# Optimization experiments

Measured on AMD Instinct MI355X. Metric: run time of the kernel, lower is better.

The kernel has to match this reference:

```python
import jax, jax.numpy as jnp
import numpy as np

EMB_DIM = 2048
N_Q_HEADS = 32
N_KV_HEADS = 8
HEAD_DIM = EMB_DIM // N_Q_HEADS  # 64
N_REP = N_Q_HEADS // N_KV_HEADS  # 4
ROPE_BASE = 10000.0


def setup_inputs() -> dict:
    key = jax.random.key(0)
    ks = jax.random.split(key, 9)
    B, T = 2, 2048
    kv_dim = HEAD_DIM * N_KV_HEADS
    s = 0.02
    return {
        "x":  jax.random.normal(ks[0], (B, T, EMB_DIM), jnp.float32),
        "Wq": jax.random.normal(ks[1], (EMB_DIM, EMB_DIM), jnp.float32) * s,
        "bq": jax.random.normal(ks[2], (EMB_DIM,), jnp.float32) * s,
        "Wk": jax.random.normal(ks[3], (kv_dim, EMB_DIM), jnp.float32) * s,
        "bk": jax.random.normal(ks[4], (kv_dim,), jnp.float32) * s,
        "Wv": jax.random.normal(ks[5], (kv_dim, EMB_DIM), jnp.float32) * s,
        "bv": jax.random.normal(ks[6], (kv_dim,), jnp.float32) * s,
        "Wo": jax.random.normal(ks[7], (EMB_DIM, EMB_DIM), jnp.float32) * s,
        "bo": jax.random.normal(ks[8], (EMB_DIM,), jnp.float32) * s,
    }


def _rope_tables(T, D, dtype):
    inv_freq = 1.0 / (ROPE_BASE ** (jnp.arange(0, D, 2, dtype=jnp.float32) / D))
    t = jnp.arange(T, dtype=jnp.float32)
    freqs = jnp.einsum("i,j->ij", t, inv_freq)          # [T, D/2]
    emb = jnp.concatenate([freqs, freqs], axis=-1)       # [T, D]
    # broadcast over batch and heads: [1, T, 1, D]
    return jnp.cos(emb)[None, :, None, :].astype(dtype), jnp.sin(emb)[None, :, None, :].astype(dtype)


def _rotate_half(x):
    x1, x2 = jnp.split(x, 2, axis=-1)
    return jnp.concatenate([-x2, x1], axis=-1)


def reference(x, Wq, bq, Wk, bk, Wv, bv, Wo, bo):
    B, T, C = x.shape
    q = (x @ Wq.T + bq).reshape(B, T, N_Q_HEADS, HEAD_DIM)
    k = (x @ Wk.T + bk).reshape(B, T, N_KV_HEADS, HEAD_DIM)
    v = (x @ Wv.T + bv).reshape(B, T, N_KV_HEADS, HEAD_DIM)

    cos, sin = _rope_tables(T, HEAD_DIM, x.dtype)
    q = q * cos + _rotate_half(q) * sin
    k = k * cos + _rotate_half(k) * sin

    q = q.transpose(0, 2, 1, 3)                          # [B, Hq, T, D]
    k = k.transpose(0, 2, 1, 3)                          # [B, Hkv, T, D]
    v = v.transpose(0, 2, 1, 3)
    # GQA: repeat_interleave kv heads to match query heads
    k = jnp.repeat(k, N_REP, axis=1)                     # [B, Hq, T, D]
    v = jnp.repeat(v, N_REP, axis=1)

    scale = 1.0 / jnp.sqrt(jnp.asarray(HEAD_DIM, x.dtype))
    att = jnp.einsum("bhqd,bhkd->bhqk", q, k) * scale    # [B, Hq, T, T]
    causal = jnp.tril(jnp.ones((T, T), dtype=bool))
    att = jnp.where(causal[None, None], att, -jnp.inf)
    att = jax.nn.softmax(att, axis=-1)

    y = jnp.einsum("bhqk,bhkd->bhqd", att, v)            # [B, Hq, T, D]
    y = y.transpose(0, 2, 1, 3).reshape(B, T, C)
    return y @ Wo.T + bo
```

## Files before the change

### kernel.cpp

```cpp
#include <hip/hip_runtime.h>
#include <hip/hip_bf16.h>
#include <math.h>


typedef __attribute__((ext_vector_type(8))) short short8;
typedef __attribute__((ext_vector_type(4))) float f32x4;

#define MFMA16(a,b,c) __builtin_amdgcn_mfma_f32_16x16x32_bf16((a),(b),(c),0,0,0)
#define QSCALE 0.18033688011112043f
#define NFREQ  (-13.28771237954945f / 32.0f)

__device__ __forceinline__ ushort f2bf(float f) {
  union { float f; unsigned u; } x; x.f = f;
  unsigned r = x.u + 0x7fffu + ((x.u >> 16) & 1u);
  return (ushort)(r >> 16);
}
__device__ __forceinline__ uint pkbf(float a, float b) {
  union { float f; unsigned u; } x, y; x.f = a; y.f = b;
  return ((x.u + 0x8000u) >> 16) | ((y.u + 0x8000u) & 0xffff0000u);
}

__device__ __forceinline__ void g2l16(const void* g, void* l) {
  __builtin_amdgcn_global_load_lds(
      (__attribute__((address_space(1))) void*)g,
      (__attribute__((address_space(3))) void*)l, 16, 0, 0);
}

__global__ void cvt_all(const float* __restrict__ x,  const float* __restrict__ wq,
                        const float* __restrict__ wk, const float* __restrict__ wv,
                        const float* __restrict__ wo,
                        ushort* __restrict__ x_bf, ushort* __restrict__ wqkv,
                        ushort* __restrict__ wo_bf) {
  int i = blockIdx.x * 256 + threadIdx.x;
  const float4* src; ushort* dst; int off;
  if (i < 2097152)      { src = (const float4*)x;  dst = x_bf;             off = i; }
  else if (i < 3145728) { src = (const float4*)wq; dst = wqkv;             off = i - 2097152; }
  else if (i < 3407872) { src = (const float4*)wk; dst = wqkv + 4194304;   off = i - 3145728; }
  else if (i < 3670016) { src = (const float4*)wv; dst = wqkv + 5242880;   off = i - 3407872; }
  else                  { src = (const float4*)wo; dst = wo_bf;            off = i - 3670016; }
  float4 v = src[off];
  ushort4 o;
  o.x = f2bf(v.x); o.y = f2bf(v.y); o.z = f2bf(v.z); o.w = f2bf(v.w);
  ((ushort4*)dst)[off] = o;
}

__global__ __launch_bounds__(256, 3)
void gemm_qkv(const ushort* __restrict__ A, const ushort* __restrict__ Bw,
              const float* __restrict__ bq, const float* __restrict__ bk,
              const float* __restrict__ bv,
              ushort* __restrict__ qr, ushort* __restrict__ kr,
              ushort* __restrict__ vt) {
  const int K = 2048;
  __shared__ ushort As[2][128*32];
  __shared__ ushort Bs[2][128*32];
  const int tid = threadIdx.x;
  const int wave = tid >> 6, lane = tid & 63;
  const int wm = wave >> 1, wn = wave & 1;
  const int quad = lane >> 4, l16 = lane & 15;
  const int swg = (l16 >> 1) & 3;
  int id = blockIdx.y * 24 + blockIdx.x;
  id = (id & 7) * 96 + (id >> 3);
  const int bx = id % 24, by = id / 24;
  const int m0 = by * 128, n0 = bx * 128;

  f32x4 acc[4][4] = {};

  auto stage = [&](int buf, int k0) {
#pragma unroll
    for (int i = 0; i < 2; ++i) {
      int cbase = (i*4 + wave) * 64;
      int p = cbase + lane;
      int row = p >> 2, pcb = p & 3;
      int cl = pcb ^ ((row >> 1) & 3);
      g2l16(A  + (size_t)(m0 + row) * K + k0 + cl * 8, As[buf] + (size_t)cbase * 8);
      g2l16(Bw + (size_t)(n0 + row) * K + k0 + cl * 8, Bs[buf] + (size_t)cbase * 8);
    }
  };

  stage(0, 0);
  for (int k0 = 0; k0 < K; k0 += 32) {
    __syncthreads();
    int cur = (k0 >> 5) & 1;
    if (k0 + 32 < K) stage(cur ^ 1, k0 + 32);

    short8 af[4], bfr[4];
#pragma unroll
    for (int mi = 0; mi < 4; ++mi)
      af[mi] = *(const short8*)(As[cur] + (wm*64 + mi*16 + l16)*32 + ((quad ^ swg) * 8));
#pragma unroll
    for (int ni = 0; ni < 4; ++ni)
      bfr[ni] = *(const short8*)(Bs[cur] + (wn*64 + ni*16 + l16)*32 + ((quad ^ swg) * 8));
#pragma unroll
    for (int mi = 0; mi < 4; ++mi)
#pragma unroll
      for (int ni = 0; ni < 4; ++ni)
        acc[mi][ni] = MFMA16(af[mi], bfr[ni], acc[mi][ni]);
  }

  const int bb = m0 >> 11;
  const int tb = (m0 & 2047) + wm*64;

  if (bx < 20) {
    const bool isq = bx < 16;
    const float scale = isq ? QSCALE : 1.0f;
#pragma unroll
    for (int ni = 0; ni < 2; ++ni) {
      int n = n0 + wn*64 + ni*16 + l16;
      int d = ni*16 + l16;
      float bias1, bias2;
      ushort* dst;
      if (isq) {
        bias1 = bq[n]; bias2 = bq[n + 32];
        dst = qr + ((size_t)(bb*32 + (n >> 6)) * 2048) * 64 + d;
      } else {
        bias1 = bk[n - 2048]; bias2 = bk[n - 2016];
        dst = kr + ((size_t)(bb*8 + ((n >> 6) - 32)) * 2048) * 64 + d;
      }
      float invf = exp2f((float)d * NFREQ);
#pragma unroll
      for (int mi = 0; mi < 4; ++mi) {
#pragma unroll
        for (int r = 0; r < 4; ++r) {
          int t = tb + mi*16 + quad*4 + r;
          float x1 = acc[mi][ni][r]   + bias1;
          float x2 = acc[mi][ni+2][r] + bias2;
          float f = (float)t * invf;
          float sn = __sinf(f), cs = __cosf(f);
          dst[(size_t)t*64]      = f2bf((x1*cs - x2*sn) * scale);
          dst[(size_t)t*64 + 32] = f2bf((x2*cs + x1*sn) * scale);
        }
      }
    }
  } else {
#pragma unroll
    for (int ni = 0; ni < 4; ++ni) {
      int n = n0 + wn*64 + ni*16 + l16;
      int d = ni*16 + l16;
      float bias = bv[n - 2560];
      ushort* dst = vt + ((size_t)(bb*8 + ((n - 2560) >> 6)) * 64 + d) * 2048;
#pragma unroll
      for (int mi = 0; mi < 4; ++mi) {
        int t = tb + mi*16 + quad*4;
        uint2 pk;
        pk.x = (uint)f2bf(acc[mi][ni][0]+bias) | ((uint)f2bf(acc[mi][ni][1]+bias) << 16);
        pk.y = (uint)f2bf(acc[mi][ni][2]+bias) | ((uint)f2bf(acc[mi][ni][3]+bias) << 16);
        *(uint2*)(dst + t) = pk;
      }
    }
  }
}

__global__ __launch_bounds__(256, 3)
void gemm128(const ushort* __restrict__ A, const ushort* __restrict__ Bw,
             const float* __restrict__ b0,
             float* __restrict__ Cout, int M, int N, int K) {
  __shared__ ushort As[2][128*32];
  __shared__ ushort Bs[2][128*32];
  const int tid = threadIdx.x;
  const int wave = tid >> 6, lane = tid & 63;
  const int wm = wave >> 1, wn = wave & 1;
  const int quad = lane >> 4, l16 = lane & 15;
  const int swg = (l16 >> 1) & 3;
  int id = blockIdx.y * 16 + blockIdx.x;
  id = (id & 7) * 64 + (id >> 3);
  const int m0 = (id / 16) * 128, n0 = (id % 16) * 128;

  f32x4 acc[4][4] = {};

  auto stage = [&](int buf, int k0) {
#pragma unroll
    for (int i = 0; i < 2; ++i) {
      int cbase = (i*4 + wave) * 64;
      int p = cbase + lane;
      int row = p >> 2, pcb = p & 3;
      int cl = pcb ^ ((row >> 1) & 3);
      g2l16(A  + (size_t)(m0 + row) * K + k0 + cl * 8, As[buf] + (size_t)cbase * 8);
      g2l16(Bw + (size_t)(n0 + row) * K + k0 + cl * 8, Bs[buf] + (size_t)cbase * 8);
    }
  };

  stage(0, 0);
  for (int k0 = 0; k0 < K; k0 += 32) {
    __syncthreads();
    int cur = (k0 >> 5) & 1;
    if (k0 + 32 < K) stage(cur ^ 1, k0 + 32);

    short8 af[4], bfr[4];
#pragma unroll
    for (int mi = 0; mi < 4; ++mi)
      af[mi] = *(const short8*)(As[cur] + (wm*64 + mi*16 + l16)*32 + ((quad ^ swg) * 8));
#pragma unroll
    for (int ni = 0; ni < 4; ++ni)
      bfr[ni] = *(const short8*)(Bs[cur] + (wn*64 + ni*16 + l16)*32 + ((quad ^ swg) * 8));
#pragma unroll
    for (int mi = 0; mi < 4; ++mi)
#pragma unroll
      for (int ni = 0; ni < 4; ++ni)
        acc[mi][ni] = MFMA16(af[mi], bfr[ni], acc[mi][ni]);
  }

#pragma unroll
  for (int ni = 0; ni < 4; ++ni) {
    int n = n0 + wn*64 + ni*16 + l16;
    float bias = b0[n];
#pragma unroll
    for (int mi = 0; mi < 4; ++mi) {
#pragma unroll
      for (int r = 0; r < 4; ++r) {
        int m = m0 + wm*64 + mi*16 + quad*4 + r;
        Cout[(size_t)m * N + n] = acc[mi][ni][r] + bias;
      }
    }
  }
}

__global__ __launch_bounds__(512, 4)
void attn(const ushort* __restrict__ Q, const ushort* __restrict__ Kb,
          const ushort* __restrict__ Vt, ushort* __restrict__ Y) {
  __shared__ ushort Ks[2][64*64];
  __shared__ ushort Vs[2][64*64];
  __shared__ ushort Ps[8*16*64];
  const int tid = threadIdx.x, wave = tid >> 6, lane = tid & 63;
  const int quad = lane >> 4, l16 = lane & 15;
  const int h = blockIdx.y, b = blockIdx.z;
  const int hk = h >> 2;
  const ushort* Qb = Q  + ((size_t)(b*32 + h)  * 2048) * 64;
  const ushort* Kg = Kb + ((size_t)(b*8 + hk) * 2048) * 64;
  const ushort* Vg = Vt + ((size_t)(b*8 + hk) * 64) * 2048;
  ushort* Pw = Ps + wave * 1024;
  const int sw = l16 & 7;

  auto stage = [&](int buf, int kt) {
    int p = tid;
    int row = p >> 3, pcb = p & 7;
    int cl = pcb ^ (row & 7);
    g2l16(Kg + (size_t)(kt*64 + row)*64 + cl*8, Ks[buf] + wave*512);
    g2l16(Vg + (size_t)row*2048 + kt*64 + cl*8, Vs[buf] + wave*512);
  };

  for (int pass = 0; pass < 2; ++pass) {
    const int qt = pass ? (15 - blockIdx.x) : blockIdx.x;
    const int q0 = qt * 128;
    const int qrow = q0 + wave*16 + l16;
    short8 qf0 = *(const short8*)(Qb + (size_t)qrow*64 + quad*8);
    short8 qf1 = *(const short8*)(Qb + (size_t)qrow*64 + 32 + quad*8);

    f32x4 o[4] = {};
    f32x4 l4 = {0.f, 0.f, 0.f, 0.f};

    __syncthreads();
    stage(0, 0);

    const int ktmax = qt*2 + 1;
    for (int kt = 0; kt <= ktmax; ++kt) {
      __syncthreads();
      int cur = kt & 1;
      if (kt < ktmax) stage(cur ^ 1, kt + 1);

      f32x4 s[4];
      __builtin_amdgcn_s_setprio(1);
#pragma unroll
      for (int kb = 0; kb < 4; ++kb) {
        const ushort* krow = Ks[cur] + (kb*16 + l16)*64;
        short8 kf0 = *(const short8*)(krow + ((quad       ^ sw) * 8));
        short8 kf1 = *(const short8*)(krow + (((4 + quad) ^ sw) * 8));
        f32x4 z = {0.f, 0.f, 0.f, 0.f};
        z = MFMA16(kf0, qf0, z);
        s[kb] = MFMA16(kf1, qf1, z);
      }
      __builtin_amdgcn_s_setprio(0);

      if (kt >= qt*2) {
        int ql = q0 + wave*16 + l16;
#pragma unroll
        for (int kb = 0; kb < 4; ++kb) {
          int key = kt*64 + kb*16 + quad*4;
#pragma unroll
          for (int r = 0; r < 4; ++r)
            if (key + r > ql) s[kb][r] = -INFINITY;
        }
      }

#pragma unroll
      for (int kb = 0; kb < 4; ++kb)
#pragma unroll
        for (int r = 0; r < 4; ++r)
          s[kb][r] = __builtin_amdgcn_exp2f(s[kb][r]);

      l4 += (s[0] + s[1]) + (s[2] + s[3]);

#pragma unroll
      for (int kb = 0; kb < 4; ++kb) {
        uint2 pk;
        pk.x = pkbf(s[kb][0], s[kb][1]);
        pk.y = pkbf(s[kb][2], s[kb][3]);
        int G = (kb*2 + (quad >> 1)) ^ sw;
        *(uint2*)((char*)Pw + l16*128 + G*16 + (quad & 1)*8) = pk;
      }

      __builtin_amdgcn_s_setprio(1);
#pragma unroll
      for (int kc = 0; kc < 2; ++kc) {
        short8 pf = *(const short8*)((char*)Pw + l16*128 + (((kc*4 + quad) ^ sw) * 16));
#pragma unroll
        for (int db = 0; db < 4; ++db) {
          const ushort* vrow = Vs[cur] + (db*16 + l16)*64;
          short8 vf = *(const short8*)(vrow + (((kc*4 + quad) ^ sw) * 8));
          o[db] = MFMA16(vf, pf, o[db]);
        }
      }
      __builtin_amdgcn_s_setprio(0);
    }

    float l = (l4[0] + l4[1]) + (l4[2] + l4[3]);
    l += __shfl_xor(l, 16);
    l += __shfl_xor(l, 32);
    float inv = 1.0f / l;

    int q = q0 + wave*16 + l16;
#pragma unroll
    for (int db = 0; db < 4; ++db) {
      size_t base = ((size_t)(b*2048 + q)) * 2048 + h*64 + db*16 + quad*4;
      ((uint*)Y)[base >> 1]       = pkbf(o[db][0]*inv, o[db][1]*inv);
      ((uint*)Y)[(base >> 1) + 1] = pkbf(o[db][2]*inv, o[db][3]*inv);
    }
  }
}

extern "C" void kernel_launch(void* const* d_in, const int* in_sizes, int n_in,
                              void* d_out, int out_size, void* d_ws, size_t ws_size,
                              hipStream_t stream) {
  (void)in_sizes; (void)n_in; (void)out_size; (void)ws_size;
  const float* x  = (const float*)d_in[0];
  const float* Wq = (const float*)d_in[1];
  const float* bq = (const float*)d_in[2];
  const float* Wk = (const float*)d_in[3];
  const float* bk = (const float*)d_in[4];
  const float* Wv = (const float*)d_in[5];
  const float* bv = (const float*)d_in[6];
  const float* Wo = (const float*)d_in[7];
  const float* bo = (const float*)d_in[8];
  float* out = (float*)d_out;

  ushort* ws    = (ushort*)d_ws;
  ushort* x_bf  = ws;
  ushort* wqkv  = x_bf + 8388608;
  ushort* wo_bf = wqkv + 6291456;
  ushort* qr    = wo_bf + 4194304;
  ushort* kr    = qr + 8388608;
  ushort* vt    = kr + 2097152;
  ushort* Y     = x_bf;

  cvt_all<<<18432, 256, 0, stream>>>(x, Wq, Wk, Wv, Wo, x_bf, wqkv, wo_bf);
  gemm_qkv<<<dim3(24, 32), 256, 0, stream>>>(x_bf, wqkv, bq, bk, bv, qr, kr, vt);
  attn<<<dim3(8, 32, 2), 512, 0, stream>>>(qr, kr, vt, Y);
  gemm128<<<dim3(16, 32), 256, 0, stream>>>(Y, wo_bf, bo, out, 4096, 2048, 2048);
}
```

Measured before the change: 286.3 us.

## Switch attention to 32x32 MFMA tiles with in-register P via permlane32 swap

Changes the attention kernel from 16x16x32 MFMA with 8 waves of 16 query rows each to 32x32x16 MFMA with 4 waves of 32 query rows each. The P matrix is no longer written to and read back from LDS. It is repacked in registers with permlane32_swap so it can feed the PV MFMA directly. Removing the LDS round trip for P and using larger MFMA tiles should cut LDS traffic and instruction count. The costs are fewer threads per block, more registers per thread (f32x16 accumulators), and lower occupancy.

```diff
diff --git a/kernel.cpp b/kernel.cpp
--- a/kernel.cpp
+++ b/kernel.cpp
@@ -5,8 +5,11 @@
 
 typedef __attribute__((ext_vector_type(8))) short short8;
 typedef __attribute__((ext_vector_type(4))) float f32x4;
+typedef __attribute__((ext_vector_type(16))) float f32x16;
+typedef __attribute__((ext_vector_type(2))) unsigned int uint2v;
 
 #define MFMA16(a,b,c) __builtin_amdgcn_mfma_f32_16x16x32_bf16((a),(b),(c),0,0,0)
+#define MFMA32(a,b,c) __builtin_amdgcn_mfma_f32_32x32x16_bf16((a),(b),(c),0,0,0)
 #define QSCALE 0.18033688011112043f
 #define NFREQ  (-13.28771237954945f / 32.0f)
 
@@ -214,39 +217,41 @@
   }
 }
 
-__global__ __launch_bounds__(512, 4)
+__global__ __launch_bounds__(256, 2)
 void attn(const ushort* __restrict__ Q, const ushort* __restrict__ Kb,
           const ushort* __restrict__ Vt, ushort* __restrict__ Y) {
   __shared__ ushort Ks[2][64*64];
   __shared__ ushort Vs[2][64*64];
-  __shared__ ushort Ps[8*16*64];
   const int tid = threadIdx.x, wave = tid >> 6, lane = tid & 63;
-  const int quad = lane >> 4, l16 = lane & 15;
+  const int l32 = lane & 31, hh = lane >> 5;
   const int h = blockIdx.y, b = blockIdx.z;
   const int hk = h >> 2;
   const ushort* Qb = Q  + ((size_t)(b*32 + h)  * 2048) * 64;
   const ushort* Kg = Kb + ((size_t)(b*8 + hk) * 2048) * 64;
   const ushort* Vg = Vt + ((size_t)(b*8 + hk) * 64) * 2048;
-  ushort* Pw = Ps + wave * 1024;
-  const int sw = l16 & 7;
 
   auto stage = [&](int buf, int kt) {
-    int p = tid;
-    int row = p >> 3, pcb = p & 7;
-    int cl = pcb ^ (row & 7);
-    g2l16(Kg + (size_t)(kt*64 + row)*64 + cl*8, Ks[buf] + wave*512);
-    g2l16(Vg + (size_t)row*2048 + kt*64 + cl*8, Vs[buf] + wave*512);
+#pragma unroll
+    for (int i = 0; i < 2; ++i) {
+      int p = i*256 + tid;
+      int row = p >> 3, pcb = p & 7;
+      int cl = pcb ^ (row & 7);
+      g2l16(Kg + (size_t)(kt*64 + row)*64 + cl*8, Ks[buf] + (size_t)p*8);
+      g2l16(Vg + (size_t)row*2048 + kt*64 + cl*8, Vs[buf] + (size_t)p*8);
+    }
   };
 
   for (int pass = 0; pass < 2; ++pass) {
     const int qt = pass ? (15 - blockIdx.x) : blockIdx.x;
     const int q0 = qt * 128;
-    const int qrow = q0 + wave*16 + l16;
-    short8 qf0 = *(const short8*)(Qb + (size_t)qrow*64 + quad*8);
-    short8 qf1 = *(const short8*)(Qb + (size_t)qrow*64 + 32 + quad*8);
-
-    f32x4 o[4] = {};
-    f32x4 l4 = {0.f, 0.f, 0.f, 0.f};
+    const int qrow = q0 + wave*32 + l32;
+    short8 qf[4];
+#pragma unroll
+    for (int ks = 0; ks < 4; ++ks)
+      qf[ks] = *(const short8*)(Qb + (size_t)qrow*64 + ks*16 + hh*8);
+
+    f32x16 o[2] = {};
+    float lsum = 0.f;
 
     __syncthreads();
     stage(0, 0);
@@ -257,72 +262,81 @@
       int cur = kt & 1;
       if (kt < ktmax) stage(cur ^ 1, kt + 1);
 
-      f32x4 s[4];
+      f32x16 s[2];
       __builtin_amdgcn_s_setprio(1);
 #pragma unroll
-      for (int kb = 0; kb < 4; ++kb) {
-        const ushort* krow = Ks[cur] + (kb*16 + l16)*64;
-        short8 kf0 = *(const short8*)(krow + ((quad       ^ sw) * 8));
-        short8 kf1 = *(const short8*)(krow + (((4 + quad) ^ sw) * 8));
-        f32x4 z = {0.f, 0.f, 0.f, 0.f};
-        z = MFMA16(kf0, qf0, z);
-        s[kb] = MFMA16(kf1, qf1, z);
+      for (int kb = 0; kb < 2; ++kb) {
+        f32x16 z = {};
+#pragma unroll
+        for (int ks = 0; ks < 4; ++ks) {
+          int row = kb*32 + l32;
+          short8 kf = *(const short8*)(Ks[cur] + row*64 + (((ks*2 + hh) ^ (row & 7)) * 8));
+          z = MFMA32(kf, qf[ks], z);
+        }
+        s[kb] = z;
       }
       __builtin_amdgcn_s_setprio(0);
 
-      if (kt >= qt*2) {
-        int ql = q0 + wave*16 + l16;
-#pragma unroll
-        for (int kb = 0; kb < 4; ++kb) {
-          int key = kt*64 + kb*16 + quad*4;
-#pragma unroll
-          for (int r = 0; r < 4; ++r)
-            if (key + r > ql) s[kb][r] = -INFINITY;
+      if (kt*64 + 63 > qrow - l32) {
+#pragma unroll
+        for (int kb = 0; kb < 2; ++kb)
+#pragma unroll
+          for (int r = 0; r < 16; ++r) {
+            int key = kt*64 + kb*32 + (r & 3) + 8*(r >> 2) + 4*hh;
+            if (key > qrow) s[kb][r] = -INFINITY;
+          }
+      }
+
+#pragma unroll
+      for (int kb = 0; kb < 2; ++kb)
+#pragma unroll
+        for (int r = 0; r < 16; ++r) {
+          s[kb][r] = __builtin_amdgcn_exp2f(s[kb][r]);
+          lsum += s[kb][r];
         }
-      }
-
-#pragma unroll
-      for (int kb = 0; kb < 4; ++kb)
-#pragma unroll
-        for (int r = 0; r < 4; ++r)
-          s[kb][r] = __builtin_amdgcn_exp2f(s[kb][r]);
-
-      l4 += (s[0] + s[1]) + (s[2] + s[3]);
-
-#pragma unroll
-      for (int kb = 0; kb < 4; ++kb) {
+
+      __builtin_amdgcn_s_setprio(1);
+#pragma unroll
+      for (int kb = 0; kb < 2; ++kb) {
+#pragma unroll
+        for (int c = 0; c < 2; ++c) {
+          int rb = c*8;
+          uint a0 = pkbf(s[kb][rb+0], s[kb][rb+1]);
+          uint b0 = pkbf(s[kb][rb+4], s[kb][rb+5]);
+          uint a1 = pkbf(s[kb][rb+2], s[kb][rb+3]);
+          uint b1 = pkbf(s[kb][rb+6], s[kb][rb+7]);
+          uint2v r0 = __builtin_amdgcn_permlane32_swap(a0, b0, false, false);
+          uint2v r1 = __builtin_amdgcn_permlane32_swap(a1, b1, false, false);
+          union { uint u[4]; short8 s8; } pa;
+          pa.u[0] = r0[0]; pa.u[1] = r1[0]; pa.u[2] = r0[1]; pa.u[3] = r1[1];
+#pragma unroll
+          for (int db = 0; db < 2; ++db) {
+            int row = db*32 + l32;
+            short8 vf = *(const short8*)(Vs[cur] + row*64 +
+                          (((kb*4 + c*2 + hh) ^ (row & 7)) * 8));
+            o[db] = MFMA32(vf, pa.s8, o[db]);
+          }
+        }
+      }
+      __builtin_amdgcn_s_setprio(0);
+    }
+
+    union { float f; uint u; } lu; lu.f = lsum;
+    uint2v lr = __builtin_amdgcn_permlane32_swap(lu.u, lu.u, false, false);
+    union { uint u; float f; } la, lb; la.u = lr[0]; lb.u = lr[1];
+    float inv = 1.0f / (la.f + lb.f);
+
+#pragma unroll
+    for (int db = 0; db < 2; ++db) {
+#pragma unroll
+      for (int g = 0; g < 4; ++g) {
+        int d = db*32 + 8*g + 4*hh;
+        size_t base = ((size_t)(b*2048 + qrow)) * 2048 + h*64 + d;
         uint2 pk;
-        pk.x = pkbf(s[kb][0], s[kb][1]);
-        pk.y = pkbf(s[kb][2], s[kb][3]);
-        int G = (kb*2 + (quad >> 1)) ^ sw;
-        *(uint2*)((char*)Pw + l16*128 + G*16 + (quad & 1)*8) = pk;
-      }
-
-      __builtin_amdgcn_s_setprio(1);
-#pragma unroll
-      for (int kc = 0; kc < 2; ++kc) {
-        short8 pf = *(const short8*)((char*)Pw + l16*128 + (((kc*4 + quad) ^ sw) * 16));
-#pragma unroll
-        for (int db = 0; db < 4; ++db) {
-          const ushort* vrow = Vs[cur] + (db*16 + l16)*64;
-          short8 vf = *(const short8*)(vrow + (((kc*4 + quad) ^ sw) * 8));
-          o[db] = MFMA16(vf, pf, o[db]);
-        }
-      }
-      __builtin_amdgcn_s_setprio(0);
-    }
-
-    float l = (l4[0] + l4[1]) + (l4[2] + l4[3]);
-    l += __shfl_xor(l, 16);
-    l += __shfl_xor(l, 32);
-    float inv = 1.0f / l;
-
-    int q = q0 + wave*16 + l16;
-#pragma unroll
-    for (int db = 0; db < 4; ++db) {
-      size_t base = ((size_t)(b*2048 + q)) * 2048 + h*64 + db*16 + quad*4;
-      ((uint*)Y)[base >> 1]       = pkbf(o[db][0]*inv, o[db][1]*inv);
-      ((uint*)Y)[(base >> 1) + 1] = pkbf(o[db][2]*inv, o[db][3]*inv);
+        pk.x = pkbf(o[db][4*g+0]*inv, o[db][4*g+1]*inv);
+        pk.y = pkbf(o[db][4*g+2]*inv, o[db][4*g+3]*inv);
+        *(uint2*)((ushort*)Y + base) = pk;
+      }
     }
   }
 }
@@ -353,6 +367,6 @@
 
   cvt_all<<<18432, 256, 0, stream>>>(x, Wq, Wk, Wv, Wo, x_bf, wqkv, wo_bf);
   gemm_qkv<<<dim3(24, 32), 256, 0, stream>>>(x_bf, wqkv, bq, bk, bv, qr, kr, vt);
-  attn<<<dim3(8, 32, 2), 512, 0, stream>>>(qr, kr, vt, Y);
+  attn<<<dim3(8, 32, 2), 256, 0, stream>>>(qr, kr, vt, Y);
   gemm128<<<dim3(16, 32), 256, 0, stream>>>(Y, wo_bf, bo, out, 4096, 2048, 2048);
 }
```

Measured after the change: 286.6 us. Within noise of the previous version (+0.1%).
